# Optimization experiments

Measured on AMD Instinct MI355X. Metric: run time of the kernel, lower is better.

## Reference

```python
import jax, jax.numpy as jnp
import numpy as np

TEMP = 0.0005

def conv1d(x, w, b):
    # x: [B, Cin, T], w: [Cout, Cin, K] -> [B, Cout, T] with SAME padding
    out = jax.lax.conv_general_dilated(x, w, (1,), 'SAME', dimension_numbers=('NCH', 'OIH', 'NCH'))
    return out + b[None, :, None]

def setup_inputs() -> dict:
    key = jax.random.key(0)
    ks = jax.random.split(key, 24)
    B, Cs, T1 = 16, 80, 1000   # spec channels / mel frames
    Ct, T2 = 512, 200          # text channels / phonemes
    Ca, G = 80, 256            # attention channels / speaker embedding
    n = lambda i, shape: jax.random.normal(ks[i], shape, jnp.float32)
    w = lambda i, shape: n(i, shape) * 0.05
    return {
        'queries': n(0, (B, Cs, T1)),
        'keys': n(1, (B, Ct, T2)),
        'mask': jnp.ones((B, T2), jnp.int32),
        'attn_prior': jax.random.uniform(ks[2], (B, T1, T2), jnp.float32),
        'g': n(3, (B, G)),
        # key_proj: Conv(Ct -> 2Ct, k=3) -> ReLU -> Conv(2Ct -> Ca, k=1)
        'wk1': w(4, (2 * Ct, Ct, 3)), 'bk1': jnp.zeros((2 * Ct,), jnp.float32),
        'wk2': w(5, (Ca, 2 * Ct, 1)), 'bk2': jnp.zeros((Ca,), jnp.float32),
        # query_proj: Conv(Cs -> 2Cs, k=3) -> ReLU -> Conv(2Cs -> Cs, k=1) -> ReLU -> Conv(Cs -> Ca, k=1)
        'wq1': w(6, (2 * Cs, Cs, 3)), 'bq1': jnp.zeros((2 * Cs,), jnp.float32),
        'wq2': w(7, (Cs, 2 * Cs, 1)), 'bq2': jnp.zeros((Cs,), jnp.float32),
        'wq3': w(8, (Ca, Cs, 1)), 'bq3': jnp.zeros((Ca,), jnp.float32),
        # speaker projections (LinearNorm): gin -> n_text_channels / n_spec_channels
        'w_kspk': w(9, (Ct, G)), 'b_kspk': jnp.zeros((Ct,), jnp.float32),
        'w_qspk': w(10, (Cs, G)), 'b_qspk': jnp.zeros((Cs,), jnp.float32),
    }

def reference(queries, keys, mask, attn_prior, g, wk1, bk1, wk2, bk2, wq1, bq1, wq2, bq2, wq3, bq3, w_kspk, b_kspk, w_qspk, b_qspk):
    # speaker conditioning: same projected vector added at every time step
    keys = keys + (g @ w_kspk.T + b_kspk)[:, :, None]
    queries = queries + (g @ w_qspk.T + b_qspk)[:, :, None]
    # projections
    k_enc = conv1d(jax.nn.relu(conv1d(keys, wk1, bk1)), wk2, bk2)              # [B, Ca, T2]
    q = jax.nn.relu(conv1d(queries, wq1, bq1))
    q = jax.nn.relu(conv1d(q, wq2, bq2))
    q_enc = conv1d(q, wq3, bq3)                                                # [B, Ca, T1]
    # squared L2 distance via GEMM trick: |q|^2 + |k|^2 - 2 q.k  (same math as broadcast diff)
    q2 = jnp.sum(q_enc * q_enc, axis=1)[:, :, None]                            # [B, T1, 1]
    k2 = jnp.sum(k_enc * k_enc, axis=1)[:, None, :]                            # [B, 1, T2]
    qk = jnp.einsum('bct,bcs->bts', q_enc, k_enc)                              # [B, T1, T2]
    attn = (-TEMP * (q2 + k2 - 2.0 * qk))[:, None]                             # [B, 1, T1, T2]
    attn = jax.nn.log_softmax(attn, axis=3) + jnp.log(attn_prior[:, None] + 1e-8)
    attn_logprob = attn
    neg_inf = jnp.where(mask[:, None, None, :] == 0, -jnp.inf, 0.0)
    attn = jax.nn.softmax(attn + neg_inf, axis=3)
    return attn, attn_logprob
```

## Files before the change

kernel.cpp:

```cpp
#include <hip/hip_runtime.h>
#include <hip/hip_bf16.h>
#include <math.h>

#define NB 16
#define CS 80
#define T1 1000
#define CT 512
#define T2 200
#define CA 80
#define GD 256
#define C2T 1024
#define C2S 160
#define TEMP_F 0.0005f
#define ENC_STR 96
#define WPITCH 388

typedef __attribute__((ext_vector_type(8))) short short8;
typedef __attribute__((ext_vector_type(4))) float floatx4;

__device__ __forceinline__ short f2bf(float x) {
    unsigned u = __builtin_bit_cast(unsigned, x);
    unsigned r = (u + 0x7fffu + ((u >> 16) & 1u)) >> 16;
    return (short)r;
}

struct KP {
    const float* queries; const float* keys; const int* mask; const float* prior; const float* g;
    const float* wk1; const float* bk1; const float* wk2; const float* bk2;
    const float* wq1; const float* bq1; const float* wq2; const float* bq2;
    const float* wq3; const float* bq3;
    const float* w_kspk; const float* b_kspk; const float* w_qspk; const float* b_qspk;
    short* wk1p; short* wq1p; short* wk2p; short* wq2p; short* wq3p;
    short* xkT; short* xqT; short* k_encT; short* q_encT; float* k2ws;
    short* kh1T; short* qh1T; float* out_attn; float* out_logp;
};

template <int COUT, int CIN, int KW, int COP, int CINP>
__device__ __forceinline__ void wpack_body(const float* __restrict__ w,
                                           short* __restrict__ wp, int bid) {
    constexpr int NC32 = CINP / 32;
    constexpr int NFRAG = (COP / 16) * KW * NC32;
    int gid = bid * 256 + threadIdx.x;
    int frag = gid >> 6, lane = gid & 63;
    if (frag >= NFRAG) return;
    int co16 = frag / (KW * NC32), rem = frag - co16 * (KW * NC32);
    int k = rem / NC32, ci32 = rem - k * NC32;
    int co = co16 * 16 + (lane & 15);
    int ci = ci32 * 32 + (lane >> 4) * 8;
    short8 v;
#pragma unroll
    for (int j = 0; j < 8; j++) {
        float f = 0.f;
        if (co < COUT && ci + j < CIN) f = w[((size_t)co * CIN + ci + j) * KW + k];
        v[j] = f2bf(f);
    }
    *(short8*)(wp + (size_t)frag * 512 + lane * 8) = v;
}

template <int COUT, int CIN, int COP, int CINP>
__device__ __forceinline__ void wpack1_body(const float* __restrict__ w,
                                            short* __restrict__ wp, int bid) {
    constexpr int NC32 = CINP / 32;
    constexpr int NFRAG = (COP / 16) * NC32;
    int gid = bid * 256 + threadIdx.x;
    int frag = gid >> 6, lane = gid & 63;
    if (frag >= NFRAG) return;
    int co16 = frag / NC32, ci32 = frag - co16 * NC32;
    int co = co16 * 16 + (lane & 15);
    int ci = ci32 * 32 + (lane >> 4) * 8;
    short8 v;
    if (co < COUT && ci + 8 <= CIN) {
        const float* src = w + (size_t)co * CIN + ci;
        float4 f0 = *(const float4*)src;
        float4 f1 = *(const float4*)(src + 4);
        v[0] = f2bf(f0.x); v[1] = f2bf(f0.y); v[2] = f2bf(f0.z); v[3] = f2bf(f0.w);
        v[4] = f2bf(f1.x); v[5] = f2bf(f1.y); v[6] = f2bf(f1.z); v[7] = f2bf(f1.w);
    } else {
#pragma unroll
        for (int j = 0; j < 8; j++) {
            float f = 0.f;
            if (co < COUT && ci + j < CIN) f = w[(size_t)co * CIN + ci + j];
            v[j] = f2bf(f);
        }
    }
    *(short8*)(wp + (size_t)frag * 512 + lane * 8) = v;
}

__device__ __forceinline__ void wpack_k1_lds(const float* __restrict__ w,
                                             short* __restrict__ wp,
                                             float* smW, int bid) {
    const int tid = threadIdx.x;
    const int co16 = bid >> 2, cq = bid & 3;
    const float* src = w + (size_t)co16 * 16 * 1536 + cq * 384;
#pragma unroll
    for (int it = 0; it < 6; it++) {
        int i = tid + it * 256;
        int row = i / 96, colv = i - row * 96;
        *(float4*)(smW + row * WPITCH + colv * 4) =
            *(const float4*)(src + (size_t)row * 1536 + colv * 4);
    }
    __syncthreads();
    const int wv = tid >> 6, lane = tid & 63;
    const int r = lane & 15, hi = lane >> 4;
#pragma unroll
    for (int fo = 0; fo < 3; fo++) {
        int f = fo * 4 + wv;
        int k = f >> 2, ci32l = f & 3;
        int frag = (co16 * 3 + k) * 16 + (cq * 4 + ci32l);
        const float* base = smW + r * WPITCH + (ci32l * 32 + hi * 8) * 3 + k;
        short8 v;
#pragma unroll
        for (int j = 0; j < 8; j++) v[j] = f2bf(base[j * 3]);
        *(short8*)(wp + (size_t)frag * 512 + lane * 8) = v;
    }
}

template <int C, int T>
__device__ __forceinline__ void addspkT_body(const float* __restrict__ in,
                                             const float* __restrict__ g,
                                             const float* __restrict__ w_spk,
                                             const float* __restrict__ b_spk,
                                             short* __restrict__ outT,
                                             float* sm, int bx, int by, int b) {
    float* spkS = sm;
    float* S = sm + 32;
    const int t0 = bx * 64, c0 = by * 32;
    const int tid = threadIdx.x;
    int cl = tid >> 3, part = tid & 7;
    int c = c0 + cl;
    float s = 0.f;
    if (c < C) {
        const float* wr = w_spk + (size_t)c * GD;
        const float* gr = g + b * GD;
        int j0 = part * 32;
#pragma unroll
        for (int j = 0; j < 32; j++) s += gr[j0 + j] * wr[j0 + j];
    }
    s += __shfl_xor(s, 1, 64); s += __shfl_xor(s, 2, 64); s += __shfl_xor(s, 4, 64);
    if (part == 0) spkS[cl] = s + ((c < C) ? b_spk[c] : 0.f);
    __syncthreads();
    for (int i = tid; i < 32 * 64; i += 256) {
        int cll = i >> 6, tl = i & 63;
        int gc = c0 + cll, gt = t0 + tl;
        float v = 0.f;
        if (gc < C && gt < T) v = in[((size_t)b * C + gc) * T + gt] + spkS[cll];
        S[cll * 65 + tl] = v;
    }
    __syncthreads();
    for (int i = tid; i < 64 * 8; i += 256) {
        int tl = i >> 3, c4 = (i & 7) * 4;
        int gt = t0 + tl, gc0 = c0 + c4;
        if (gt < T) {
            if (gc0 + 3 < C) {
                ushort4 o;
                o.x = (unsigned short)f2bf(S[(c4 + 0) * 65 + tl]);
                o.y = (unsigned short)f2bf(S[(c4 + 1) * 65 + tl]);
                o.z = (unsigned short)f2bf(S[(c4 + 2) * 65 + tl]);
                o.w = (unsigned short)f2bf(S[(c4 + 3) * 65 + tl]);
                *(ushort4*)(outT + ((size_t)b * T + gt) * C + gc0) = o;
            } else {
#pragma unroll
                for (int q = 0; q < 4; q++)
                    if (gc0 + q < C)
                        outT[((size_t)b * T + gt) * C + gc0 + q] = f2bf(S[(c4 + q) * 65 + tl]);
            }
        }
    }
}

__global__ __launch_bounds__(256) void prep_kernel(KP p) {
    __shared__ __align__(16) float smP[16 * WPITCH];
    int bid = blockIdx.x;
    if (bid < 256) { wpack_k1_lds(p.wk1, p.wk1p, smP, bid); return; }
    bid -= 256;
    if (bid < 27) { wpack_body<C2S, CS, 3, 192, 96>(p.wq1, p.wq1p, bid); return; }
    bid -= 27;
    if (bid < 40) { wpack1_body<CA, C2T, 80, 1024>(p.wk2, p.wk2p, bid); return; }
    bid -= 40;
    if (bid < 7) { wpack1_body<CA, C2S, 80, 160>(p.wq2, p.wq2p, bid); return; }
    bid -= 7;
    if (bid < 4) { wpack1_body<CA, CS, 80, 96>(p.wq3, p.wq3p, bid); return; }
    bid -= 4;
    if (bid < 1024) {
        int bx = bid & 3, by = (bid >> 2) & 15, b = bid >> 6;
        addspkT_body<CT, T2>(p.keys, p.g, p.w_kspk, p.b_kspk, p.xkT, smP, bx, by, b);
        return;
    }
    bid -= 1024;
    {
        int bx = bid & 15, by = (bid >> 4) % 3, b = bid / 48;
        addspkT_body<CS, T1>(p.queries, p.g, p.w_qspk, p.b_qspk, p.xqT, smP, bx, by, b);
    }
}

template <int CIN, int COUT, int T, int KW, bool RELU, int CICH, int NC32T>
__device__ __forceinline__ void conv_body(const short* __restrict__ xT,
                                          const short* __restrict__ wp,
                                          const float* __restrict__ bias,
                                          short* __restrict__ outT,
                                          short* Xs, int bx, int by, int b) {
    constexpr int TT = 128, COT = 64;
    constexpr int PAD = KW / 2;
    constexpr int XROWS = TT + KW - 1;
    constexpr int PITCH = CICH + 8;
    constexpr int NPC = CICH / 8;
    constexpr int NC32 = CICH / 32;
    constexpr int CINP = NC32T * 32;
    constexpr int NCHK = CINP / CICH;
    constexpr int NPIECE = XROWS * NPC;
    constexpr int NLD = (NPIECE + 255) / 256;

    const int t0 = bx * TT, co0 = by * COT;
    const int tid = threadIdx.x, wave = tid >> 6, lane = tid & 63;
    const int quad = lane >> 4, l16 = lane & 15;
    const int wt = wave * 32;
    const int co16_0 = co0 >> 4;
    const short* xb = xT + (size_t)b * T * CIN;

    floatx4 acc[4][2];
#pragma unroll
    for (int mi = 0; mi < 4; mi++)
#pragma unroll
        for (int ni = 0; ni < 2; ni++) acc[mi][ni] = (floatx4){0.f, 0.f, 0.f, 0.f};

    for (int i = tid; i < NPIECE; i += 256) {
        int r = i / NPC, pp = i - r * NPC;
        int t = t0 + r - PAD, ci = pp * 8;
        uint4 v = {0u, 0u, 0u, 0u};
        if ((unsigned)t < (unsigned)T && ci + 8 <= CIN)
            v = *(const uint4*)(xb + (size_t)t * CIN + ci);
        *(uint4*)(Xs + r * PITCH + pp * 8) = v;
    }
    __syncthreads();

    for (int kc = 0; kc < NCHK; kc++) {
        uint4 tmp[NLD];
        if (NCHK > 1 && kc + 1 < NCHK) {
            int ci0n = (kc + 1) * CICH;
#pragma unroll
            for (int ld = 0; ld < NLD; ld++) {
                int i = tid + ld * 256;
                tmp[ld] = (uint4){0u, 0u, 0u, 0u};
                if (i < NPIECE) {
                    int r = i / NPC, pp = i - r * NPC;
                    int t = t0 + r - PAD, ci = ci0n + pp * 8;
                    if ((unsigned)t < (unsigned)T && ci + 8 <= CIN)
                        tmp[ld] = *(const uint4*)(xb + (size_t)t * CIN + ci);
                }
            }
        }
        const short* Xb = Xs + (NCHK > 1 ? (kc & 1) : 0) * XROWS * PITCH;
#pragma unroll
        for (int k = 0; k < KW; k++) {
#pragma unroll
            for (int kk = 0; kk < NC32; kk++) {
                int ci32 = kc * NC32 + kk;
                short8 a[4];
#pragma unroll
                for (int mi = 0; mi < 4; mi++)
                    a[mi] = *(const short8*)(wp +
                        ((size_t)((co16_0 + mi) * KW + k) * NC32T + ci32) * 512 + lane * 8);
#pragma unroll
                for (int ni = 0; ni < 2; ni++) {
                    short8 bb = *(const short8*)(Xb + (wt + ni * 16 + l16 + k) * PITCH +
                                                 kk * 32 + quad * 8);
#pragma unroll
                    for (int mi = 0; mi < 4; mi++)
                        acc[mi][ni] = __builtin_amdgcn_mfma_f32_16x16x32_bf16(a[mi], bb,
                                                                              acc[mi][ni], 0, 0, 0);
                }
            }
        }
        if (NCHK > 1 && kc + 1 < NCHK) {
            short* Xn = Xs + ((kc + 1) & 1) * XROWS * PITCH;
#pragma unroll
            for (int ld = 0; ld < NLD; ld++) {
                int i = tid + ld * 256;
                if (i < NPIECE) {
                    int r = i / NPC, pp = i - r * NPC;
                    *(uint4*)(Xn + r * PITCH + pp * 8) = tmp[ld];
                }
            }
            __syncthreads();
        }
    }
#pragma unroll
    for (int mi = 0; mi < 4; mi++) {
        int cb = co0 + mi * 16 + quad * 4;
        if (cb < COUT) {
            float4 bv = *(const float4*)(bias + cb);
#pragma unroll
            for (int ni = 0; ni < 2; ni++) {
                int t = t0 + wt + ni * 16 + l16;
                if (t < T) {
                    float v0 = acc[mi][ni][0] + bv.x, v1 = acc[mi][ni][1] + bv.y;
                    float v2 = acc[mi][ni][2] + bv.z, v3 = acc[mi][ni][3] + bv.w;
                    if (RELU) {
                        v0 = fmaxf(v0, 0.f); v1 = fmaxf(v1, 0.f);
                        v2 = fmaxf(v2, 0.f); v3 = fmaxf(v3, 0.f);
                    }
                    ushort4 o;
                    o.x = (unsigned short)f2bf(v0); o.y = (unsigned short)f2bf(v1);
                    o.z = (unsigned short)f2bf(v2); o.w = (unsigned short)f2bf(v3);
                    *(ushort4*)(outT + ((size_t)b * T + t) * COUT + cb) = o;
                }
            }
        }
    }
}

__global__ __launch_bounds__(256, 2) void conv_kernel(KP p) {
    __shared__ __align__(16) short sm[18720];
    int bid = blockIdx.x;
    if (bid < 512) {
        int bx = bid & 1, by = (bid >> 1) & 15, b = bid >> 5;
        conv_body<CT, C2T, T2, 3, true, 64, 16>(p.xkT, p.wk1p, p.bk1, p.kh1T, sm, bx, by, b);
    } else {
        int r = bid - 512;
        int bx = r & 7, by = (r >> 3) % 3, b = r / 24;
        conv_body<CS, C2S, T1, 3, true, 96, 3>(p.xqT, p.wq1p, p.bq1, p.qh1T, sm, bx, by, b);
    }
}

__device__ __forceinline__ void kgemm_body(const short* __restrict__ xT,
                                           const short* __restrict__ wp,
                                           const float* __restrict__ bias,
                                           short* __restrict__ outT,
                                           float* __restrict__ k2ws,
                                           short* sm, int bid) {
    constexpr int K = 1024, KCH = 128, PITCH = 136, NPC = 16, NCHK = 8;
    const int n0 = bid * 64;
    const int tid = threadIdx.x, wave = tid >> 6, lane = tid & 63;
    const int quad = lane >> 4, l16 = lane & 15;
    floatx4 acc[5];
#pragma unroll
    for (int mi = 0; mi < 5; mi++) acc[mi] = (floatx4){0.f, 0.f, 0.f, 0.f};

    for (int i = tid; i < 64 * NPC; i += 256) {
        int r = i / NPC, pp = i - r * NPC;
        *(uint4*)(sm + r * PITCH + pp * 8) = *(const uint4*)(xT + (size_t)(n0 + r) * K + pp * 8);
    }
    __syncthreads();
    for (int kc = 0; kc < NCHK; kc++) {
        uint4 tmp[4];
        if (kc + 1 < NCHK) {
            int ci0 = (kc + 1) * KCH;
#pragma unroll
            for (int ld = 0; ld < 4; ld++) {
                int i = tid + ld * 256;
                int r = i / NPC, pp = i - r * NPC;
                tmp[ld] = *(const uint4*)(xT + (size_t)(n0 + r) * K + ci0 + pp * 8);
            }
        }
        const short* Xb = sm + (kc & 1) * 64 * PITCH;
#pragma unroll
        for (int kk = 0; kk < 4; kk++) {
            int ci32 = kc * 4 + kk;
            short8 bb = *(const short8*)(Xb + (wave * 16 + l16) * PITCH + kk * 32 + quad * 8);
#pragma unroll
            for (int mi = 0; mi < 5; mi++) {
                short8 a = *(const short8*)(wp + ((size_t)(mi * 32 + ci32)) * 512 + lane * 8);
                acc[mi] = __builtin_amdgcn_mfma_f32_16x16x32_bf16(a, bb, acc[mi], 0, 0, 0);
            }
        }
        if (kc + 1 < NCHK) {
            short* Xn = sm + ((kc + 1) & 1) * 64 * PITCH;
#pragma unroll
            for (int ld = 0; ld < 4; ld++) {
                int i = tid + ld * 256;
                int r = i / NPC, pp = i - r * NPC;
                *(uint4*)(Xn + r * PITCH + pp * 8) = tmp[ld];
            }
            __syncthreads();
        }
    }
    int n = n0 + wave * 16 + l16;
    float sq = 0.f;
#pragma unroll
    for (int mi = 0; mi < 5; mi++) {
        int cb = mi * 16 + quad * 4;
        float4 bv = *(const float4*)(bias + cb);
        float v0 = acc[mi][0] + bv.x, v1 = acc[mi][1] + bv.y;
        float v2 = acc[mi][2] + bv.z, v3 = acc[mi][3] + bv.w;
        sq += v0 * v0 + v1 * v1 + v2 * v2 + v3 * v3;
        ushort4 o;
        o.x = (unsigned short)f2bf(v0); o.y = (unsigned short)f2bf(v1);
        o.z = (unsigned short)f2bf(v2); o.w = (unsigned short)f2bf(v3);
        *(ushort4*)(outT + (size_t)n * ENC_STR + cb) = o;
    }
    if (quad < 2) *(uint4*)(outT + (size_t)n * ENC_STR + 80 + quad * 8) = (uint4){0u, 0u, 0u, 0u};
    sq += __shfl_xor(sq, 16, 64);
    sq += __shfl_xor(sq, 32, 64);
    if (quad == 0) k2ws[n] = sq;
}

__device__ __forceinline__ void qconv23_body(const short* __restrict__ h1,
                                             const short* __restrict__ w2p,
                                             const float* __restrict__ b2,
                                             const short* __restrict__ w3p,
                                             const float* __restrict__ b3,
                                             short* __restrict__ outT, short* sm, int bid) {
    constexpr int K1 = 160, P1 = 168, NPC1 = 20, P3 = 104;
    short* Xs = sm;
    short* Hs = sm + 64 * P1;
    const int n0 = bid * 64;
    const int tid = threadIdx.x, wave = tid >> 6, lane = tid & 63;
    const int quad = lane >> 4, l16 = lane & 15;

    for (int i = tid; i < 64 * NPC1; i += 256) {
        int r = i / NPC1, pp = i - r * NPC1;
        *(uint4*)(Xs + r * P1 + pp * 8) = *(const uint4*)(h1 + (size_t)(n0 + r) * K1 + pp * 8);
    }
    if (tid < 128) *(uint4*)(Hs + (tid >> 1) * P3 + 80 + (tid & 1) * 8) = (uint4){0u, 0u, 0u, 0u};
    __syncthreads();

    floatx4 acc[5];
#pragma unroll
    for (int mi = 0; mi < 5; mi++) acc[mi] = (floatx4){0.f, 0.f, 0.f, 0.f};
#pragma unroll
    for (int kk = 0; kk < 5; kk++) {
        short8 bb = *(const short8*)(Xs + (wave * 16 + l16) * P1 + kk * 32 + quad * 8);
#pragma unroll
        for (int mi = 0; mi < 5; mi++) {
            short8 a = *(const short8*)(w2p + ((size_t)(mi * 5 + kk)) * 512 + lane * 8);
            acc[mi] = __builtin_amdgcn_mfma_f32_16x16x32_bf16(a, bb, acc[mi], 0, 0, 0);
        }
    }
#pragma unroll
    for (int mi = 0; mi < 5; mi++) {
        int cb = mi * 16 + quad * 4;
        float4 bv = *(const float4*)(b2 + cb);
        ushort4 o;
        o.x = (unsigned short)f2bf(fmaxf(acc[mi][0] + bv.x, 0.f));
        o.y = (unsigned short)f2bf(fmaxf(acc[mi][1] + bv.y, 0.f));
        o.z = (unsigned short)f2bf(fmaxf(acc[mi][2] + bv.z, 0.f));
        o.w = (unsigned short)f2bf(fmaxf(acc[mi][3] + bv.w, 0.f));
        *(ushort4*)(Hs + (wave * 16 + l16) * P3 + cb) = o;
    }
    __syncthreads();

    floatx4 acc3[5];
#pragma unroll
    for (int mi = 0; mi < 5; mi++) acc3[mi] = (floatx4){0.f, 0.f, 0.f, 0.f};
#pragma unroll
    for (int kk = 0; kk < 3; kk++) {
        short8 bb = *(const short8*)(Hs + (wave * 16 + l16) * P3 + kk * 32 + quad * 8);
#pragma unroll
        for (int mi = 0; mi < 5; mi++) {
            short8 a = *(const short8*)(w3p + ((size_t)(mi * 3 + kk)) * 512 + lane * 8);
            acc3[mi] = __builtin_amdgcn_mfma_f32_16x16x32_bf16(a, bb, acc3[mi], 0, 0, 0);
        }
    }
    int n = n0 + wave * 16 + l16;
#pragma unroll
    for (int mi = 0; mi < 5; mi++) {
        int cb = mi * 16 + quad * 4;
        float4 bv = *(const float4*)(b3 + cb);
        ushort4 o;
        o.x = (unsigned short)f2bf(acc3[mi][0] + bv.x);
        o.y = (unsigned short)f2bf(acc3[mi][1] + bv.y);
        o.z = (unsigned short)f2bf(acc3[mi][2] + bv.z);
        o.w = (unsigned short)f2bf(acc3[mi][3] + bv.w);
        *(ushort4*)(outT + (size_t)n * ENC_STR + cb) = o;
    }
    if (quad < 2) *(uint4*)(outT + (size_t)n * ENC_STR + 80 + quad * 8) = (uint4){0u, 0u, 0u, 0u};
}

__global__ __launch_bounds__(256, 2) void gemm_kernel(KP p) {
    __shared__ __align__(16) short sm[17408];
    int bid = blockIdx.x;
    if (bid < 50) kgemm_body(p.kh1T, p.wk2p, p.bk2, p.k_encT, p.k2ws, sm, bid);
    else qconv23_body(p.qh1T, p.wq2p, p.bq2, p.wq3p, p.bq3, p.q_encT, sm, bid - 50);
}

__device__ __forceinline__ float rmax16(float v) {
#pragma unroll
    for (int o = 1; o < 16; o <<= 1) v = fmaxf(v, __shfl_xor(v, o, 64));
    return v;
}
__device__ __forceinline__ float rsum16(float v) {
#pragma unroll
    for (int o = 1; o < 16; o <<= 1) v += __shfl_xor(v, o, 64);
    return v;
}

__global__ __launch_bounds__(256) void attn_kernel(KP p) {
    const int t10 = blockIdx.x * 64, b = blockIdx.y;
    const int tid = threadIdx.x, wave = tid >> 6, lane = tid & 63;
    const int quad = lane >> 4, l16 = lane & 15;

    float k2v[13]; int mskv[13];
#pragma unroll
    for (int n = 0; n < 13; n++) {
        int t2 = n * 16 + l16, t2c = t2 < T2 ? t2 : T2 - 1;
        k2v[n] = p.k2ws[b * T2 + t2c];
        mskv[n] = (t2 < T2) ? p.mask[b * T2 + t2] : 0;
    }
    const int t1base = t10 + wave * 16 + quad * 4;
    float pr[4][13];
#pragma unroll
    for (int r = 0; r < 4; r++) {
        int t1 = t1base + r, t1c = t1 < T1 ? t1 : T1 - 1;
#pragma unroll
        for (int n = 0; n < 13; n++) {
            int t2 = n * 16 + l16, t2c = t2 < T2 ? t2 : T2 - 1;
            pr[r][n] = p.prior[((size_t)b * T1 + t1c) * T2 + t2c];
        }
    }

    floatx4 acc[13];
#pragma unroll
    for (int n = 0; n < 13; n++) acc[n] = (floatx4){0.f, 0.f, 0.f, 0.f};
    const short* qb = p.q_encT + ((size_t)(b * T1 + t10 + wave * 16 + l16)) * ENC_STR + quad * 8;
    const short* kb = p.k_encT + ((size_t)(b * T2 + l16)) * ENC_STR + quad * 8;
#pragma unroll
    for (int kk = 0; kk < 3; kk++) {
        short8 a = *(const short8*)(qb + kk * 32);
#pragma unroll
        for (int n = 0; n < 13; n++) {
            short8 bb = *(const short8*)(kb + (size_t)n * 16 * ENC_STR + kk * 32);
            acc[n] = __builtin_amdgcn_mfma_f32_16x16x32_bf16(a, bb, acc[n], 0, 0, 0);
        }
    }

#pragma unroll
    for (int r = 0; r < 4; r++) {
        int t1 = t1base + r;
        bool t1ok = t1 < T1;
        float s[13], u[13];
        float mx = -INFINITY, mxu = -INFINITY;
#pragma unroll
        for (int n = 0; n < 13; n++) {
            int t2 = n * 16 + l16;
            float sv = (t2 < T2) ? TEMP_F * (2.f * acc[n][r] - k2v[n]) : -INFINITY;
            s[n] = sv;
            float uv = (t2 < T2) ? sv + __logf(pr[r][n] + 1e-8f) : -INFINITY;
            u[n] = uv;
            mx = fmaxf(mx, sv);
            mxu = fmaxf(mxu, (mskv[n] != 0) ? uv : -INFINITY);
        }
        float m = rmax16(mx);
        float m2 = rmax16(mxu);
        float se = 0.f, se2 = 0.f;
        float e2v[13];
#pragma unroll
        for (int n = 0; n < 13; n++) {
            se += (s[n] == -INFINITY) ? 0.f : __expf(s[n] - m);
            float e2 = (mskv[n] != 0) ? __expf(u[n] - m2) : 0.f;
            e2v[n] = e2;
            se2 += e2;
        }
        float logZ = __logf(rsum16(se));
        float invZ2 = 1.f / rsum16(se2);
        if (t1ok) {
#pragma unroll
            for (int n = 0; n < 13; n++) {
                int t2 = n * 16 + l16;
                if (t2 < T2) {
                    size_t o = ((size_t)b * T1 + t1) * T2 + t2;
                    p.out_attn[o] = e2v[n] * invZ2;
                    p.out_logp[o] = u[n] - m - logZ;
                }
            }
        }
    }
}

extern "C" void kernel_launch(void* const* d_in, const int* in_sizes, int n_in,
                              void* d_out, int out_size, void* d_ws, size_t ws_size,
                              hipStream_t stream) {
    KP p;
    p.queries = (const float*)d_in[0];
    p.keys    = (const float*)d_in[1];
    p.mask    = (const int*)d_in[2];
    p.prior   = (const float*)d_in[3];
    p.g       = (const float*)d_in[4];
    p.wk1 = (const float*)d_in[5];  p.bk1 = (const float*)d_in[6];
    p.wk2 = (const float*)d_in[7];  p.bk2 = (const float*)d_in[8];
    p.wq1 = (const float*)d_in[9];  p.bq1 = (const float*)d_in[10];
    p.wq2 = (const float*)d_in[11]; p.bq2 = (const float*)d_in[12];
    p.wq3 = (const float*)d_in[13]; p.bq3 = (const float*)d_in[14];
    p.w_kspk = (const float*)d_in[15]; p.b_kspk = (const float*)d_in[16];
    p.w_qspk = (const float*)d_in[17]; p.b_qspk = (const float*)d_in[18];

    short* wsS = (short*)d_ws;
    p.xkT   = wsS;
    p.xqT   = wsS + 1638400;
    p.wk1p  = wsS + 2918400;
    p.wq1p  = wsS + 4491264;
    p.wk2p  = wsS + 4546560;
    p.wq2p  = wsS + 4628480;
    p.wq3p  = wsS + 4641280;
    p.k_encT = wsS + 4648960;
    p.q_encT = wsS + 4957696;
    p.k2ws  = (float*)d_ws + 3248384;
    short* doS = (short*)d_out;
    p.kh1T = doS;
    p.qh1T = doS + 3276800;
    p.out_attn = (float*)d_out;
    p.out_logp = (float*)d_out + (size_t)NB * T1 * T2;

    prep_kernel<<<dim3(2126), dim3(256), 0, stream>>>(p);
    conv_kernel<<<dim3(896), dim3(256), 0, stream>>>(p);
    gemm_kernel<<<dim3(300), dim3(256), 0, stream>>>(p);
    attn_kernel<<<dim3(16, NB), dim3(256), 0, stream>>>(p);
}
```

Before: 190.7 us.

## Restructure speaker-add transpose tiles for vectorized loads and fewer blocks

Replaces the generic add-speaker transpose with specialized key and query bodies. Each block covers all channels for a time tile, computes the speaker projection once with float4 dot products, and writes bf16 rows with 16-byte stores through an LDS transpose. This cuts the prep grid from 2126 to 798 blocks and removes the redundant projection recomputation across channel tiles. Separately, the conv and gemm kernels raise their launch_bounds occupancy hint from 2 to 3, which may force register spills.

```diff
diff --git a/kernel.cpp b/kernel.cpp
--- a/kernel.cpp
+++ b/kernel.cpp
@@ -115,62 +115,145 @@
     }
 }
 
-template <int C, int T>
-__device__ __forceinline__ void addspkT_body(const float* __restrict__ in,
+__device__ __forceinline__ void addspkK_body(const float* __restrict__ in,
                                              const float* __restrict__ g,
                                              const float* __restrict__ w_spk,
                                              const float* __restrict__ b_spk,
                                              short* __restrict__ outT,
-                                             float* sm, int bx, int by, int b) {
+                                             float* sm, int b, int t0) {
     float* spkS = sm;
-    float* S = sm + 32;
-    const int t0 = bx * 64, c0 = by * 32;
+    short* XT = (short*)(sm + 512);
     const int tid = threadIdx.x;
-    int cl = tid >> 3, part = tid & 7;
-    int c = c0 + cl;
-    float s = 0.f;
-    if (c < C) {
-        const float* wr = w_spk + (size_t)c * GD;
-        const float* gr = g + b * GD;
-        int j0 = part * 32;
-#pragma unroll
-        for (int j = 0; j < 32; j++) s += gr[j0 + j] * wr[j0 + j];
-    }
-    s += __shfl_xor(s, 1, 64); s += __shfl_xor(s, 2, 64); s += __shfl_xor(s, 4, 64);
-    if (part == 0) spkS[cl] = s + ((c < C) ? b_spk[c] : 0.f);
-    __syncthreads();
-    for (int i = tid; i < 32 * 64; i += 256) {
-        int cll = i >> 6, tl = i & 63;
-        int gc = c0 + cll, gt = t0 + tl;
-        float v = 0.f;
-        if (gc < C && gt < T) v = in[((size_t)b * C + gc) * T + gt] + spkS[cll];
-        S[cll * 65 + tl] = v;
-    }
-    __syncthreads();
-    for (int i = tid; i < 64 * 8; i += 256) {
-        int tl = i >> 3, c4 = (i & 7) * 4;
-        int gt = t0 + tl, gc0 = c0 + c4;
-        if (gt < T) {
-            if (gc0 + 3 < C) {
-                ushort4 o;
-                o.x = (unsigned short)f2bf(S[(c4 + 0) * 65 + tl]);
-                o.y = (unsigned short)f2bf(S[(c4 + 1) * 65 + tl]);
-                o.z = (unsigned short)f2bf(S[(c4 + 2) * 65 + tl]);
-                o.w = (unsigned short)f2bf(S[(c4 + 3) * 65 + tl]);
-                *(ushort4*)(outT + ((size_t)b * T + gt) * C + gc0) = o;
-            } else {
-#pragma unroll
-                for (int q = 0; q < 4; q++)
-                    if (gc0 + q < C)
-                        outT[((size_t)b * T + gt) * C + gc0 + q] = f2bf(S[(c4 + q) * 65 + tl]);
+    const float* gr = g + b * GD;
+    {
+        int c0 = tid * 2;
+        const float* w0 = w_spk + (size_t)c0 * GD;
+        float s0 = 0.f, s1 = 0.f;
+#pragma unroll 8
+        for (int j = 0; j < GD; j += 4) {
+            float4 gv = *(const float4*)(gr + j);
+            float4 a0 = *(const float4*)(w0 + j);
+            float4 a1 = *(const float4*)(w0 + GD + j);
+            s0 += a0.x * gv.x + a0.y * gv.y + a0.z * gv.z + a0.w * gv.w;
+            s1 += a1.x * gv.x + a1.y * gv.y + a1.z * gv.z + a1.w * gv.w;
+        }
+        spkS[c0] = s0 + b_spk[c0];
+        spkS[c0 + 1] = s1 + b_spk[c0 + 1];
+    }
+    __syncthreads();
+    const bool safe = (t0 + 16 <= T2);
+#pragma unroll
+    for (int it = 0; it < 8; it++) {
+        int i = tid + it * 256;
+        int c = i >> 2, q = i & 3;
+        const float* src = in + ((size_t)b * CT + c) * T2 + t0 + q * 4;
+        float sv = spkS[c];
+        short* dst = XT + c * 18 + q * 4;
+        if (safe) {
+            float4 v = *(const float4*)src;
+            dst[0] = f2bf(v.x + sv); dst[1] = f2bf(v.y + sv);
+            dst[2] = f2bf(v.z + sv); dst[3] = f2bf(v.w + sv);
+        } else {
+#pragma unroll
+            for (int j = 0; j < 4; j++) {
+                int t = t0 + q * 4 + j;
+                dst[j] = f2bf((t < T2) ? src[j] + sv : 0.f);
+            }
+        }
+    }
+    __syncthreads();
+    const int wv = tid >> 6, lane = tid & 63;
+    const int tl = lane & 15, cg = lane >> 4;
+    if (t0 + tl < T2) {
+        short* orow = outT + ((size_t)b * T2 + t0 + tl) * CT;
+#pragma unroll
+        for (int ci = 0; ci < 4; ci++) {
+            int c0 = wv * 128 + ci * 32 + cg * 8;
+            short8 v;
+#pragma unroll
+            for (int k = 0; k < 8; k++) v[k] = XT[(c0 + k) * 18 + tl];
+            *(short8*)(orow + c0) = v;
+        }
+    }
+}
+
+__device__ __forceinline__ void addspkQ_body(const float* __restrict__ in,
+                                             const float* __restrict__ g,
+                                             const float* __restrict__ w_spk,
+                                             const float* __restrict__ b_spk,
+                                             short* __restrict__ outT,
+                                             float* sm, int b, int t0) {
+    float* spkS = sm;
+    short* XT = (short*)(sm + 80);
+    const int tid = threadIdx.x;
+    const float* gr = g + b * GD;
+    if (tid < CS) {
+        const float* w0 = w_spk + (size_t)tid * GD;
+        float s0 = 0.f;
+#pragma unroll 8
+        for (int j = 0; j < GD; j += 4) {
+            float4 gv = *(const float4*)(gr + j);
+            float4 a0 = *(const float4*)(w0 + j);
+            s0 += a0.x * gv.x + a0.y * gv.y + a0.z * gv.z + a0.w * gv.w;
+        }
+        spkS[tid] = s0 + b_spk[tid];
+    }
+    __syncthreads();
+    const bool safe = (t0 + 64 <= T1);
+#pragma unroll
+    for (int it = 0; it < 5; it++) {
+        int i = tid + it * 256;
+        int c = i >> 4, q = i & 15;
+        const float* src = in + ((size_t)b * CS + c) * T1 + t0 + q * 4;
+        float sv = spkS[c];
+        short* dst = XT + c * 66 + q * 4;
+        if (safe) {
+            float4 v = *(const float4*)src;
+            dst[0] = f2bf(v.x + sv); dst[1] = f2bf(v.y + sv);
+            dst[2] = f2bf(v.z + sv); dst[3] = f2bf(v.w + sv);
+        } else {
+#pragma unroll
+            for (int j = 0; j < 4; j++) {
+                int t = t0 + q * 4 + j;
+                dst[j] = f2bf((t < T1) ? src[j] + sv : 0.f);
+            }
+        }
+    }
+    __syncthreads();
+    const int wv = tid >> 6, lane = tid & 63;
+    const int tl = wv * 16 + (lane & 15), cg = lane >> 4;
+    int t = t0 + tl;
+    if (t < T1) {
+        short* orow = outT + ((size_t)b * T1 + t) * CS;
+#pragma unroll
+        for (int ci = 0; ci < 3; ci++) {
+            int cgt = ci * 4 + cg;
+            if (cgt < 10) {
+                int c0 = cgt * 8;
+                short8 v;
+#pragma unroll
+                for (int k = 0; k < 8; k++) v[k] = XT[(c0 + k) * 66 + tl];
+                *(short8*)(orow + c0) = v;
             }
         }
     }
 }
 
 __global__ __launch_bounds__(256) void prep_kernel(KP p) {
-    __shared__ __align__(16) float smP[16 * WPITCH];
+    __shared__ __align__(16) float smP[6208];
     int bid = blockIdx.x;
+    if (bid < 208) {
+        int b = bid / 13, tt = bid - b * 13;
+        addspkK_body(p.keys, p.g, p.w_kspk, p.b_kspk, p.xkT, smP, b, tt * 16);
+        return;
+    }
+    bid -= 208;
+    if (bid < 256) {
+        int b = bid >> 4, tt = bid & 15;
+        addspkQ_body(p.queries, p.g, p.w_qspk, p.b_qspk, p.xqT, smP, b, tt * 64);
+        return;
+    }
+    bid -= 256;
     if (bid < 256) { wpack_k1_lds(p.wk1, p.wk1p, smP, bid); return; }
     bid -= 256;
     if (bid < 27) { wpack_body<C2S, CS, 3, 192, 96>(p.wq1, p.wq1p, bid); return; }
@@ -179,18 +262,7 @@
     bid -= 40;
     if (bid < 7) { wpack1_body<CA, C2S, 80, 160>(p.wq2, p.wq2p, bid); return; }
     bid -= 7;
-    if (bid < 4) { wpack1_body<CA, CS, 80, 96>(p.wq3, p.wq3p, bid); return; }
-    bid -= 4;
-    if (bid < 1024) {
-        int bx = bid & 3, by = (bid >> 2) & 15, b = bid >> 6;
-        addspkT_body<CT, T2>(p.keys, p.g, p.w_kspk, p.b_kspk, p.xkT, smP, bx, by, b);
-        return;
-    }
-    bid -= 1024;
-    {
-        int bx = bid & 15, by = (bid >> 4) % 3, b = bid / 48;
-        addspkT_body<CS, T1>(p.queries, p.g, p.w_qspk, p.b_qspk, p.xqT, smP, bx, by, b);
-    }
+    wpack1_body<CA, CS, 80, 96>(p.wq3, p.wq3p, bid);
 }
 
 template <int CIN, int COUT, int T, int KW, bool RELU, int CICH, int NC32T>
@@ -309,7 +381,7 @@
     }
 }
 
-__global__ __launch_bounds__(256, 2) void conv_kernel(KP p) {
+__global__ __launch_bounds__(256, 3) void conv_kernel(KP p) {
     __shared__ __align__(16) short sm[18720];
     int bid = blockIdx.x;
     if (bid < 512) {
@@ -466,7 +538,7 @@
     if (quad < 2) *(uint4*)(outT + (size_t)n * ENC_STR + 80 + quad * 8) = (uint4){0u, 0u, 0u, 0u};
 }
 
-__global__ __launch_bounds__(256, 2) void gemm_kernel(KP p) {
+__global__ __launch_bounds__(256, 3) void gemm_kernel(KP p) {
     __shared__ __align__(16) short sm[17408];
     int bid = blockIdx.x;
     if (bid < 50) kgemm_body(p.kh1T, p.wk2p, p.bk2, p.k_encT, p.k2ws, sm, bid);
@@ -600,7 +672,7 @@
     p.out_attn = (float*)d_out;
     p.out_logp = (float*)d_out + (size_t)NB * T1 * T2;
 
-    prep_kernel<<<dim3(2126), dim3(256), 0, stream>>>(p);
+    prep_kernel<<<dim3(798), dim3(256), 0, stream>>>(p);
     conv_kernel<<<dim3(896), dim3(256), 0, stream>>>(p);
     gemm_kernel<<<dim3(300), dim3(256), 0, stream>>>(p);
     attn_kernel<<<dim3(16, NB), dim3(256), 0, stream>>>(p);
```

Result: slower. 195.2 us (+2.4%).
